# Kernel optimization log

Measured on AMD Instinct MI355X. Metric: run time of the kernel, lower is better.

Reference implementation:

```python
import jax, jax.numpy as jnp
import numpy as np

N_EMBD = 1024
N_HEAD = 16


def setup_inputs() -> dict:
    key = jax.random.key(0)
    ks = jax.random.split(key, 9)
    s = 1.0 / np.sqrt(N_EMBD)
    d = {
        "x": jax.random.normal(ks[0], (4, 2048, N_EMBD), dtype=jnp.float32),
        "Wq": jax.random.normal(ks[1], (N_EMBD, N_EMBD), dtype=jnp.float32) * s,
        "bq": jnp.zeros((N_EMBD,), dtype=jnp.float32),
        "Wk": jax.random.normal(ks[2], (N_EMBD, N_EMBD), dtype=jnp.float32) * s,
        "bk": jnp.zeros((N_EMBD,), dtype=jnp.float32),
        "Wv": jax.random.normal(ks[3], (N_EMBD, N_EMBD), dtype=jnp.float32) * s,
        "bv": jnp.zeros((N_EMBD,), dtype=jnp.float32),
        "Wp": jax.random.normal(ks[4], (N_EMBD, N_EMBD), dtype=jnp.float32) * s,
        "bp": jnp.zeros((N_EMBD,), dtype=jnp.float32),
    }
    return d


def reference(x, Wq, bq, Wk, bk, Wv, bv, Wp, bp):
    B, T, C = x.shape
    H = N_HEAD
    D = C // H  # head dim
    # QKV projections -> [B, H, T, D]
    def split_heads(y):
        return y.reshape(B, T, H, D).transpose(0, 2, 1, 3)
    q = split_heads(x @ Wq + bq)
    k = split_heads(x @ Wk + bk)
    v = split_heads(x @ Wv + bv)
    # full (non-causal) attention, scaled by 1/sqrt(D)
    att = jnp.einsum("bhtd,bhsd->bhts", q, k) * (1.0 / np.sqrt(D))
    att = jax.nn.softmax(att, axis=-1)  # dropout is identity (p=0 / eval)
    out = jnp.einsum("bhts,bhsd->bhtd", att, v)
    out = out.transpose(0, 2, 1, 3).reshape(B, T, C)
    return out @ Wp + bp
```

## Files before the change

### kernel.cpp

```cpp
#include <hip/hip_runtime.h>
#include <math.h>

#define B_ 4
#define T_ 2048
#define C_ 1024
#define H_ 16
#define D_ 64
#define M_ (B_ * T_)

#define QSCALE 0.18033688011112042f

using bf16x8 = __attribute__((ext_vector_type(8))) short;
using f32x4  = __attribute__((ext_vector_type(4))) float;

__device__ __forceinline__ unsigned short f2bf(float f) {
  unsigned u = __float_as_uint(f);
  unsigned r = u + 0x7FFFu + ((u >> 16) & 1u);
  return (unsigned short)(r >> 16);
}
__device__ __forceinline__ float bf2f(unsigned short h) {
  return __uint_as_float(((unsigned)h) << 16);
}
__device__ __forceinline__ unsigned cvtpk_bf16(float lo, float hi) {
  unsigned r;
  asm volatile("v_cvt_pk_bf16_f32 %0, %1, %2" : "=v"(r) : "v"(lo), "v"(hi));
  return r;
}

__global__ __launch_bounds__(256) void conv_x(const float* __restrict__ x,
                                              unsigned short* __restrict__ hi,
                                              unsigned short* __restrict__ lo) {
  const size_t i = ((size_t)blockIdx.x * 256 + threadIdx.x) * 4;
  const float4 v = *(const float4*)&x[i];
  ushort4 h, l;
  h.x = f2bf(v.x); l.x = f2bf(v.x - bf2f(h.x));
  h.y = f2bf(v.y); l.y = f2bf(v.y - bf2f(h.y));
  h.z = f2bf(v.z); l.z = f2bf(v.z - bf2f(h.z));
  h.w = f2bf(v.w); l.w = f2bf(v.w - bf2f(h.w));
  *(ushort4*)&hi[i] = h;
  *(ushort4*)&lo[i] = l;
}

__global__ __launch_bounds__(256) void conv_wT(const float* __restrict__ W,
                                               unsigned short* __restrict__ hi,
                                               unsigned short* __restrict__ lo,
                                               int n_off) {
  __shared__ float t[64][65];
  const int k0 = blockIdx.y * 64, n0 = blockIdx.x * 64;
  const int lr = threadIdx.x >> 4;
  const int lc4 = (threadIdx.x & 15) * 4;
#pragma unroll
  for (int i = 0; i < 4; ++i) {
    const int r = lr + 16 * i;
    const float4 v = *(const float4*)&W[(size_t)(k0 + r) * 1024 + n0 + lc4];
    t[r][lc4 + 0] = v.x; t[r][lc4 + 1] = v.y;
    t[r][lc4 + 2] = v.z; t[r][lc4 + 3] = v.w;
  }
  __syncthreads();
#pragma unroll
  for (int i = 0; i < 4; ++i) {
    const int nr = lr + 16 * i;
    ushort4 h, l;
    float a0 = t[lc4 + 0][nr], a1 = t[lc4 + 1][nr];
    float a2 = t[lc4 + 2][nr], a3 = t[lc4 + 3][nr];
    h.x = f2bf(a0); l.x = f2bf(a0 - bf2f(h.x));
    h.y = f2bf(a1); l.y = f2bf(a1 - bf2f(h.y));
    h.z = f2bf(a2); l.z = f2bf(a2 - bf2f(h.z));
    h.w = f2bf(a3); l.w = f2bf(a3 - bf2f(h.w));
    const size_t o = (size_t)(n_off + n0 + nr) * 1024 + k0 + lc4;
    *(ushort4*)&hi[o] = h;
    *(ushort4*)&lo[o] = l;
  }
}

template <int MODE>
__global__ __launch_bounds__(256) void gemm_mfma(
    const unsigned short* __restrict__ Ahi, const unsigned short* __restrict__ Alo,
    const unsigned short* __restrict__ Bhi, const unsigned short* __restrict__ Blo,
    const float* __restrict__ bias0, const float* __restrict__ bias1,
    const float* __restrict__ bias2,
    void* P0, void* P1, void* P2, void* P3, void* P4, void* P5) {
  __shared__ __align__(16) unsigned short AhS[128 * 32];
  __shared__ __align__(16) unsigned short AlS[128 * 32];
  __shared__ __align__(16) unsigned short BhS[128 * 32];
  __shared__ __align__(16) unsigned short BlS[128 * 32];

  const int tid = threadIdx.x;
  const int lane = tid & 63;
  const int wid = tid >> 6;

  const int GX = (MODE == 1) ? 24 : 8;
  const int nwg = GX * 64;
  int lin = blockIdx.x + blockIdx.y * GX;
  lin = (lin & 7) * (nwg >> 3) + (lin >> 3);
  const int m0 = (lin / GX) * 128, n0 = (lin % GX) * 128;

  const int wm = (wid >> 1) * 64, wn = (wid & 1) * 64;

  f32x4 acc[4][4] = {};

  const int srow = lane >> 2;
  const int sc = lane & 3;
  const int fr = lane & 15;
  const int q = lane >> 4;

  for (int k0 = 0; k0 < 1024; k0 += 32) {
    __syncthreads();
#pragma unroll
    for (int c = 0; c < 2; ++c) {
      const int chunk = wid * 2 + c;
      const int row = chunk * 16 + srow;
      const int kch = sc ^ ((row >> 1) & 3);
      const size_t ao = (size_t)(m0 + row) * 1024 + k0 + kch * 8;
      const size_t bo = (size_t)(n0 + row) * 1024 + k0 + kch * 8;
      __builtin_amdgcn_global_load_lds(
          (const __attribute__((address_space(1))) void*)(Ahi + ao),
          (__attribute__((address_space(3))) void*)(AhS + chunk * 512), 16, 0, 0);
      __builtin_amdgcn_global_load_lds(
          (const __attribute__((address_space(1))) void*)(Alo + ao),
          (__attribute__((address_space(3))) void*)(AlS + chunk * 512), 16, 0, 0);
      __builtin_amdgcn_global_load_lds(
          (const __attribute__((address_space(1))) void*)(Bhi + bo),
          (__attribute__((address_space(3))) void*)(BhS + chunk * 512), 16, 0, 0);
      __builtin_amdgcn_global_load_lds(
          (const __attribute__((address_space(1))) void*)(Blo + bo),
          (__attribute__((address_space(3))) void*)(BlS + chunk * 512), 16, 0, 0);
    }
    __syncthreads();

    bf16x8 afh[4], bfh[4], afl[4], bfl[4];
#pragma unroll
    for (int i = 0; i < 4; ++i) {
      const int arow = wm + i * 16 + fr;
      const int aoff = arow * 32 + (q ^ ((arow >> 1) & 3)) * 8;
      afh[i] = *(const bf16x8*)(AhS + aoff);
      const int brow = wn + i * 16 + fr;
      const int boff = brow * 32 + (q ^ ((brow >> 1) & 3)) * 8;
      bfh[i] = *(const bf16x8*)(BhS + boff);
    }
#pragma unroll
    for (int i = 0; i < 4; ++i)
#pragma unroll
      for (int j = 0; j < 4; ++j)
        acc[i][j] = __builtin_amdgcn_mfma_f32_16x16x32_bf16(afh[i], bfh[j], acc[i][j], 0, 0, 0);
#pragma unroll
    for (int i = 0; i < 4; ++i) {
      const int brow = wn + i * 16 + fr;
      bfl[i] = *(const bf16x8*)(BlS + brow * 32 + (q ^ ((brow >> 1) & 3)) * 8);
    }
#pragma unroll
    for (int i = 0; i < 4; ++i)
#pragma unroll
      for (int j = 0; j < 4; ++j)
        acc[i][j] = __builtin_amdgcn_mfma_f32_16x16x32_bf16(afh[i], bfl[j], acc[i][j], 0, 0, 0);
#pragma unroll
    for (int i = 0; i < 4; ++i) {
      const int arow = wm + i * 16 + fr;
      afl[i] = *(const bf16x8*)(AlS + arow * 32 + (q ^ ((arow >> 1) & 3)) * 8);
    }
#pragma unroll
    for (int i = 0; i < 4; ++i)
#pragma unroll
      for (int j = 0; j < 4; ++j)
        acc[i][j] = __builtin_amdgcn_mfma_f32_16x16x32_bf16(afl[i], bfh[j], acc[i][j], 0, 0, 0);
  }

  if (MODE == 0) {
    float* out = (float*)P0;
#pragma unroll
    for (int i = 0; i < 4; ++i)
#pragma unroll
      for (int j = 0; j < 4; ++j)
#pragma unroll
        for (int r = 0; r < 4; ++r) {
          const int m = m0 + wm + i * 16 + q * 4 + r;
          const int n = n0 + wn + j * 16 + fr;
          out[(size_t)m * 1024 + n] = acc[i][j][r] + bias0[n];
        }
  } else {
#pragma unroll
    for (int i = 0; i < 4; ++i) {
#pragma unroll
      for (int j = 0; j < 4; ++j) {
        const int n = n0 + wn + j * 16 + fr;
        const int seg = n >> 10, ww = n & 1023, h = ww >> 6, d = ww & 63;
        const float bv = ((seg == 0) ? bias0 : (seg == 1) ? bias1 : bias2)[ww];
        const int mb = m0 + wm + i * 16 + q * 4;
        const int b = mb >> 11, t0 = mb & 2047;
        unsigned short hv[4], lv[4];
#pragma unroll
        for (int r = 0; r < 4; ++r) {
          float v = acc[i][j][r] + bv;
          if (seg == 0) v *= QSCALE;
          hv[r] = f2bf(v);
          lv[r] = f2bf(v - bf2f(hv[r]));
        }
        if (seg == 2) {
          const size_t o = (((size_t)b * H_ + h) * D_ + d) * T_ + t0;
          ushort4 h4, l4;
          h4.x = hv[0]; h4.y = hv[1]; h4.z = hv[2]; h4.w = hv[3];
          l4.x = lv[0]; l4.y = lv[1]; l4.z = lv[2]; l4.w = lv[3];
          *(ushort4*)&((unsigned short*)P4)[o] = h4;
          *(ushort4*)&((unsigned short*)P5)[o] = l4;
        } else {
          unsigned short* Hq = (unsigned short*)((seg == 0) ? P0 : P2);
          unsigned short* Lq = (unsigned short*)((seg == 0) ? P1 : P3);
          const size_t ob = ((size_t)b * H_ + h) * T_;
#pragma unroll
          for (int r = 0; r < 4; ++r) {
            const size_t o = (ob + t0 + r) * D_ + d;
            Hq[o] = hv[r];
            Lq[o] = lv[r];
          }
        }
      }
    }
  }
}

__global__ __launch_bounds__(256) void flash_mfma(
    const unsigned short* __restrict__ Qhi, const unsigned short* __restrict__ Qlo,
    const unsigned short* __restrict__ Khi, const unsigned short* __restrict__ Klo,
    const unsigned short* __restrict__ Vthi, const unsigned short* __restrict__ Vtlo,
    unsigned short* __restrict__ chi, unsigned short* __restrict__ clo) {
  __shared__ __align__(16) unsigned short KhiS[2][64 * 64];
  __shared__ __align__(16) unsigned short KloS[2][64 * 64];
  __shared__ __align__(16) unsigned short VhiS[2][64 * 64];
  __shared__ __align__(16) unsigned short VloS[2][64 * 64];
  __shared__ __align__(16) unsigned short PsT[4][32 * 64];

  const int tid = threadIdx.x;
  const int lane = tid & 63;
  const int w = tid >> 6;

  int lin = blockIdx.x + blockIdx.y * 16;
  lin = (lin & 7) * 128 + (lin >> 3);
  const int bh = lin >> 4;
  const int q0 = (lin & 15) * 128;

  const int b = bh >> 4, h = bh & 15;
  const int fr = lane & 15, q = lane >> 4;

  const size_t kbase = (size_t)bh * T_ * D_;
  const size_t vbase = (size_t)bh * D_ * T_;

  const int ci0 = w * 128 + lane;
  const int srow0 = ci0 >> 3, sslot0 = ci0 & 7;
  const int skch0 = sslot0 ^ (srow0 & 7);
  const int ci1 = ci0 + 64;
  const int srow1 = ci1 >> 3, sslot1 = ci1 & 7;
  const int skch1 = sslot1 ^ (srow1 & 7);
  const int ldsb0 = (w * 128) * 8;
  const int ldsb1 = (w * 128 + 64) * 8;

#define STAGE_TILE(buf, s0)                                                      \
  do {                                                                           \
    const unsigned short* k0p = Khi + kbase + (size_t)((s0) + srow0) * D_ + skch0 * 8; \
    const unsigned short* k1p = Klo + kbase + (size_t)((s0) + srow0) * D_ + skch0 * 8; \
    const unsigned short* v0p = Vthi + vbase + (size_t)srow0 * T_ + (s0) + skch0 * 8;  \
    const unsigned short* v1p = Vtlo + vbase + (size_t)srow0 * T_ + (s0) + skch0 * 8;  \
    __builtin_amdgcn_global_load_lds(                                            \
        (const __attribute__((address_space(1))) void*)k0p,                      \
        (__attribute__((address_space(3))) void*)(KhiS[buf] + ldsb0), 16, 0, 0); \
    __builtin_amdgcn_global_load_lds(                                            \
        (const __attribute__((address_space(1))) void*)k1p,                      \
        (__attribute__((address_space(3))) void*)(KloS[buf] + ldsb0), 16, 0, 0); \
    __builtin_amdgcn_global_load_lds(                                            \
        (const __attribute__((address_space(1))) void*)v0p,                      \
        (__attribute__((address_space(3))) void*)(VhiS[buf] + ldsb0), 16, 0, 0); \
    __builtin_amdgcn_global_load_lds(                                            \
        (const __attribute__((address_space(1))) void*)v1p,                      \
        (__attribute__((address_space(3))) void*)(VloS[buf] + ldsb0), 16, 0, 0); \
    const unsigned short* k2p = Khi + kbase + (size_t)((s0) + srow1) * D_ + skch1 * 8; \
    const unsigned short* k3p = Klo + kbase + (size_t)((s0) + srow1) * D_ + skch1 * 8; \
    const unsigned short* v2p = Vthi + vbase + (size_t)srow1 * T_ + (s0) + skch1 * 8;  \
    const unsigned short* v3p = Vtlo + vbase + (size_t)srow1 * T_ + (s0) + skch1 * 8;  \
    __builtin_amdgcn_global_load_lds(                                            \
        (const __attribute__((address_space(1))) void*)k2p,                      \
        (__attribute__((address_space(3))) void*)(KhiS[buf] + ldsb1), 16, 0, 0); \
    __builtin_amdgcn_global_load_lds(                                            \
        (const __attribute__((address_space(1))) void*)k3p,                      \
        (__attribute__((address_space(3))) void*)(KloS[buf] + ldsb1), 16, 0, 0); \
    __builtin_amdgcn_global_load_lds(                                            \
        (const __attribute__((address_space(1))) void*)v2p,                      \
        (__attribute__((address_space(3))) void*)(VhiS[buf] + ldsb1), 16, 0, 0); \
    __builtin_amdgcn_global_load_lds(                                            \
        (const __attribute__((address_space(1))) void*)v3p,                      \
        (__attribute__((address_space(3))) void*)(VloS[buf] + ldsb1), 16, 0, 0); \
  } while (0)

  bf16x8 qhi[2][2], qlo[2][2];
#pragma unroll
  for (int g = 0; g < 2; ++g)
#pragma unroll
    for (int ks = 0; ks < 2; ++ks) {
      const size_t a = kbase + (size_t)(q0 + w * 32 + g * 16 + fr) * D_ + ks * 32 + q * 8;
      qhi[g][ks] = *(const bf16x8*)(Qhi + a);
      qlo[g][ks] = *(const bf16x8*)(Qlo + a);
    }

  unsigned short* psw = &PsT[w][0];

  f32x4 accO[4][2] = {};
  float lsum[2] = {};

  STAGE_TILE(0, 0);

  int cur = 0;
  for (int s0 = 0; s0 < T_; s0 += 64) {
    const bool more = (s0 + 64) < T_;
    if (more) {
      STAGE_TILE(cur ^ 1, s0 + 64);
      asm volatile("s_waitcnt vmcnt(8)" ::: "memory");
    } else {
      asm volatile("s_waitcnt vmcnt(0)" ::: "memory");
    }
    __builtin_amdgcn_sched_barrier(0);
    asm volatile("s_barrier" ::: "memory");
    __builtin_amdgcn_sched_barrier(0);

    const unsigned short* KhS = KhiS[cur];
    const unsigned short* KlS = KloS[cur];
    const unsigned short* VhS = VhiS[cur];
    const unsigned short* VlS = VloS[cur];

    f32x4 accS[4][2] = {};
#pragma unroll
    for (int sj = 0; sj < 4; ++sj) {
      bf16x8 khf[2], klf[2];
#pragma unroll
      for (int ks = 0; ks < 2; ++ks) {
        const int rs = sj * 16 + fr;
        const int off = rs * 64 + ((ks * 4 + q) ^ (rs & 7)) * 8;
        khf[ks] = *(const bf16x8*)(KhS + off);
        klf[ks] = *(const bf16x8*)(KlS + off);
      }
#pragma unroll
      for (int g = 0; g < 2; ++g)
#pragma unroll
        for (int ks = 0; ks < 2; ++ks) {
          accS[sj][g] = __builtin_amdgcn_mfma_f32_16x16x32_bf16(khf[ks], qhi[g][ks], accS[sj][g], 0, 0, 0);
          accS[sj][g] = __builtin_amdgcn_mfma_f32_16x16x32_bf16(khf[ks], qlo[g][ks], accS[sj][g], 0, 0, 0);
          accS[sj][g] = __builtin_amdgcn_mfma_f32_16x16x32_bf16(klf[ks], qhi[g][ks], accS[sj][g], 0, 0, 0);
        }
    }

#pragma unroll
    for (int g = 0; g < 2; ++g) {
      const int qc = g * 16 + fr;
#pragma unroll
      for (int sj = 0; sj < 4; ++sj) {
        const float p0 = __builtin_amdgcn_exp2f(accS[sj][g][0]);
        const float p1 = __builtin_amdgcn_exp2f(accS[sj][g][1]);
        const float p2 = __builtin_amdgcn_exp2f(accS[sj][g][2]);
        const float p3 = __builtin_amdgcn_exp2f(accS[sj][g][3]);
        lsum[g] += (p0 + p1) + (p2 + p3);
        uint2 pk;
        pk.x = cvtpk_bf16(p0, p1);
        pk.y = cvtpk_bf16(p2, p3);
        const int off = (qc * 128 + sj * 32 + q * 8) ^ ((fr & 7) << 4);
        *(uint2*)((char*)psw + off) = pk;
      }
    }

    asm volatile("s_waitcnt lgkmcnt(0)" ::: "memory");
    __builtin_amdgcn_sched_barrier(0);

    bf16x8 pb[2][2];
#pragma unroll
    for (int g = 0; g < 2; ++g)
#pragma unroll
      for (int ks = 0; ks < 2; ++ks) {
        const int off = ((g * 16 + fr) * 128 + ks * 64 + q * 16) ^ ((fr & 7) << 4);
        pb[g][ks] = *(const bf16x8*)((char*)psw + off);
      }
#pragma unroll
    for (int j = 0; j < 4; ++j) {
      bf16x8 vh[2], vl[2];
#pragma unroll
      for (int ks = 0; ks < 2; ++ks) {
        const int rd = j * 16 + fr;
        const int off = rd * 64 + ((ks * 4 + q) ^ (rd & 7)) * 8;
        vh[ks] = *(const bf16x8*)(VhS + off);
        vl[ks] = *(const bf16x8*)(VlS + off);
      }
#pragma unroll
      for (int g = 0; g < 2; ++g)
#pragma unroll
        for (int ks = 0; ks < 2; ++ks) {
          accO[j][g] = __builtin_amdgcn_mfma_f32_16x16x32_bf16(vh[ks], pb[g][ks], accO[j][g], 0, 0, 0);
          accO[j][g] = __builtin_amdgcn_mfma_f32_16x16x32_bf16(vl[ks], pb[g][ks], accO[j][g], 0, 0, 0);
        }
    }

    __builtin_amdgcn_sched_barrier(0);
    asm volatile("s_barrier" ::: "memory");
    __builtin_amdgcn_sched_barrier(0);
    cur ^= 1;
  }

#pragma unroll
  for (int g = 0; g < 2; ++g) {
    float rs = lsum[g];
    rs += __shfl_xor(rs, 16);
    rs += __shfl_xor(rs, 32);
    const float inv = 1.0f / rs;
    const int t = q0 + w * 32 + g * 16 + fr;
    const size_t rowb = ((size_t)b * T_ + t) * C_ + h * D_;
#pragma unroll
    for (int j = 0; j < 4; ++j) {
      ushort4 h4, l4;
      float v0 = accO[j][g][0] * inv, v1 = accO[j][g][1] * inv;
      float v2 = accO[j][g][2] * inv, v3 = accO[j][g][3] * inv;
      h4.x = f2bf(v0); l4.x = f2bf(v0 - bf2f(h4.x));
      h4.y = f2bf(v1); l4.y = f2bf(v1 - bf2f(h4.y));
      h4.z = f2bf(v2); l4.z = f2bf(v2 - bf2f(h4.z));
      h4.w = f2bf(v3); l4.w = f2bf(v3 - bf2f(h4.w));
      const size_t idx = rowb + j * 16 + q * 4;
      *(ushort4*)&chi[idx] = h4;
      *(ushort4*)&clo[idx] = l4;
    }
  }
#undef STAGE_TILE
}

extern "C" void kernel_launch(void* const* d_in, const int* in_sizes, int n_in,
                              void* d_out, int out_size, void* d_ws,
                              size_t ws_size, hipStream_t stream) {
  const float* x = (const float*)d_in[0];
  const float* Wq = (const float*)d_in[1];
  const float* bq = (const float*)d_in[2];
  const float* Wk = (const float*)d_in[3];
  const float* bk = (const float*)d_in[4];
  const float* Wv = (const float*)d_in[5];
  const float* bv = (const float*)d_in[6];
  const float* Wp = (const float*)d_in[7];
  const float* bp = (const float*)d_in[8];
  float* out = (float*)d_out;

  char* w = (char*)d_ws;
  unsigned short* xhi = (unsigned short*)w;     w += (size_t)M_ * C_ * 2;
  unsigned short* xlo = (unsigned short*)w;     w += (size_t)M_ * C_ * 2;
  unsigned short* Wqkv_hi = (unsigned short*)w; w += (size_t)3 * C_ * C_ * 2;
  unsigned short* Wqkv_lo = (unsigned short*)w; w += (size_t)3 * C_ * C_ * 2;
  unsigned short* Wp_hi = (unsigned short*)w;   w += (size_t)C_ * C_ * 2;
  unsigned short* Wp_lo = (unsigned short*)w;   w += (size_t)C_ * C_ * 2;
  unsigned short* Qhi = (unsigned short*)w;     w += (size_t)M_ * C_ * 2;
  unsigned short* Qlo = (unsigned short*)w;     w += (size_t)M_ * C_ * 2;
  unsigned short* Khi = (unsigned short*)w;     w += (size_t)M_ * C_ * 2;
  unsigned short* Klo = (unsigned short*)w;     w += (size_t)M_ * C_ * 2;
  unsigned short* Vthi = (unsigned short*)w;    w += (size_t)M_ * C_ * 2;
  unsigned short* Vtlo = (unsigned short*)w;    w += (size_t)M_ * C_ * 2;
  unsigned short* chi = (unsigned short*)w;     w += (size_t)M_ * C_ * 2;
  unsigned short* clo = (unsigned short*)w;     w += (size_t)M_ * C_ * 2;

  const dim3 blk(256);

  conv_x<<<dim3((M_ * C_) / (4 * 256)), blk, 0, stream>>>(x, xhi, xlo);
  conv_wT<<<dim3(16, 16), blk, 0, stream>>>(Wq, Wqkv_hi, Wqkv_lo, 0);
  conv_wT<<<dim3(16, 16), blk, 0, stream>>>(Wk, Wqkv_hi, Wqkv_lo, 1024);
  conv_wT<<<dim3(16, 16), blk, 0, stream>>>(Wv, Wqkv_hi, Wqkv_lo, 2048);
  conv_wT<<<dim3(16, 16), blk, 0, stream>>>(Wp, Wp_hi, Wp_lo, 0);

  gemm_mfma<1><<<dim3(3072 / 128, M_ / 128), blk, 0, stream>>>(
      xhi, xlo, Wqkv_hi, Wqkv_lo, bq, bk, bv,
      Qhi, Qlo, Khi, Klo, Vthi, Vtlo);

  flash_mfma<<<dim3(T_ / 128, B_ * H_), blk, 0, stream>>>(
      Qhi, Qlo, Khi, Klo, Vthi, Vtlo, chi, clo);

  gemm_mfma<0><<<dim3(1024 / 128, M_ / 128), blk, 0, stream>>>(
      chi, clo, Wp_hi, Wp_lo, bp, bp, bp,
      out, nullptr, nullptr, nullptr, nullptr, nullptr);

  (void)in_sizes; (void)n_in; (void)out_size; (void)ws_size;
}
```

Before: 493.1 us.

## Double-buffer GEMM LDS staging with 256x128 tiles and 8-wave blocks

Reworks the split-bf16 GEMM kernel so each 512-thread block computes a 256x128 output tile. The next K-slice is prefetched into a second LDS buffer while the current one is consumed, with explicit vmcnt waits, barriers and MFMA priority raising. This is meant to hide global-to-LDS load latency behind MFMA work and to raise operand reuse per block. In exchange, LDS use roughly doubles per block, which can lower occupancy, and the extra barriers per K-step add synchronisation cost.

```diff
diff --git a/kernel.cpp b/kernel.cpp
--- a/kernel.cpp
+++ b/kernel.cpp
@@ -74,95 +74,137 @@
 }
 
 template <int MODE>
-__global__ __launch_bounds__(256) void gemm_mfma(
+__global__ __launch_bounds__(512, 2) void gemm_mfma(
     const unsigned short* __restrict__ Ahi, const unsigned short* __restrict__ Alo,
     const unsigned short* __restrict__ Bhi, const unsigned short* __restrict__ Blo,
     const float* __restrict__ bias0, const float* __restrict__ bias1,
     const float* __restrict__ bias2,
     void* P0, void* P1, void* P2, void* P3, void* P4, void* P5) {
-  __shared__ __align__(16) unsigned short AhS[128 * 32];
-  __shared__ __align__(16) unsigned short AlS[128 * 32];
-  __shared__ __align__(16) unsigned short BhS[128 * 32];
-  __shared__ __align__(16) unsigned short BlS[128 * 32];
+  __shared__ __align__(16) unsigned short AhS[2][256 * 32];
+  __shared__ __align__(16) unsigned short AlS[2][256 * 32];
+  __shared__ __align__(16) unsigned short BhS[2][128 * 32];
+  __shared__ __align__(16) unsigned short BlS[2][128 * 32];
 
   const int tid = threadIdx.x;
   const int lane = tid & 63;
-  const int wid = tid >> 6;
+  const int w = tid >> 6;
 
   const int GX = (MODE == 1) ? 24 : 8;
-  const int nwg = GX * 64;
+  const int nwg = GX * 32;
   int lin = blockIdx.x + blockIdx.y * GX;
   lin = (lin & 7) * (nwg >> 3) + (lin >> 3);
-  const int m0 = (lin / GX) * 128, n0 = (lin % GX) * 128;
-
-  const int wm = (wid >> 1) * 64, wn = (wid & 1) * 64;
+  const int m0 = (lin / GX) * 256, n0 = (lin % GX) * 128;
+
+  const int wm = (w >> 1) * 64, wn = (w & 1) * 64;
+  const int fr = lane & 15, q = lane >> 4;
+
+  const int ciA0 = w * 64 + lane;
+  const int ciA1 = ciA0 + 512;
+  const int rA0 = ciA0 >> 2, sA0 = (ciA0 & 3) ^ ((rA0 >> 1) & 3);
+  const int rA1 = ciA1 >> 2, sA1 = (ciA1 & 3) ^ ((rA1 >> 1) & 3);
+  const int rB = rA0, sB = sA0;
 
   f32x4 acc[4][4] = {};
 
-  const int srow = lane >> 2;
-  const int sc = lane & 3;
-  const int fr = lane & 15;
-  const int q = lane >> 4;
+  auto stage = [&](int buf, int kk) {
+    const size_t oa0 = (size_t)(m0 + rA0) * 1024 + kk + sA0 * 8;
+    const size_t oa1 = (size_t)(m0 + rA1) * 1024 + kk + sA1 * 8;
+    const size_t ob  = (size_t)(n0 + rB) * 1024 + kk + sB * 8;
+    __builtin_amdgcn_global_load_lds(
+        (const __attribute__((address_space(1))) void*)(Ahi + oa0),
+        (__attribute__((address_space(3))) void*)(&AhS[buf][ciA0 * 8]), 16, 0, 0);
+    __builtin_amdgcn_global_load_lds(
+        (const __attribute__((address_space(1))) void*)(Alo + oa0),
+        (__attribute__((address_space(3))) void*)(&AlS[buf][ciA0 * 8]), 16, 0, 0);
+    __builtin_amdgcn_global_load_lds(
+        (const __attribute__((address_space(1))) void*)(Ahi + oa1),
+        (__attribute__((address_space(3))) void*)(&AhS[buf][ciA1 * 8]), 16, 0, 0);
+    __builtin_amdgcn_global_load_lds(
+        (const __attribute__((address_space(1))) void*)(Alo + oa1),
+        (__attribute__((address_space(3))) void*)(&AlS[buf][ciA1 * 8]), 16, 0, 0);
+    __builtin_amdgcn_global_load_lds(
+        (const __attribute__((address_space(1))) void*)(Bhi + ob),
+        (__attribute__((address_space(3))) void*)(&BhS[buf][ciA0 * 8]), 16, 0, 0);
+    __builtin_amdgcn_global_load_lds(
+        (const __attribute__((address_space(1))) void*)(Blo + ob),
+        (__attribute__((address_space(3))) void*)(&BlS[buf][ciA0 * 8]), 16, 0, 0);
+  };
+
+  auto frag = [&](const unsigned short* arr, int row) {
+    return *(const bf16x8*)(arr + row * 32 + ((q ^ ((row >> 1) & 3)) * 8));
+  };
+
+  stage(0, 0);
+  int cur = 0;
 
   for (int k0 = 0; k0 < 1024; k0 += 32) {
-    __syncthreads();
-#pragma unroll
-    for (int c = 0; c < 2; ++c) {
-      const int chunk = wid * 2 + c;
-      const int row = chunk * 16 + srow;
-      const int kch = sc ^ ((row >> 1) & 3);
-      const size_t ao = (size_t)(m0 + row) * 1024 + k0 + kch * 8;
-      const size_t bo = (size_t)(n0 + row) * 1024 + k0 + kch * 8;
-      __builtin_amdgcn_global_load_lds(
-          (const __attribute__((address_space(1))) void*)(Ahi + ao),
-          (__attribute__((address_space(3))) void*)(AhS + chunk * 512), 16, 0, 0);
-      __builtin_amdgcn_global_load_lds(
-          (const __attribute__((address_space(1))) void*)(Alo + ao),
-          (__attribute__((address_space(3))) void*)(AlS + chunk * 512), 16, 0, 0);
-      __builtin_amdgcn_global_load_lds(
-          (const __attribute__((address_space(1))) void*)(Bhi + bo),
-          (__attribute__((address_space(3))) void*)(BhS + chunk * 512), 16, 0, 0);
-      __builtin_amdgcn_global_load_lds(
-          (const __attribute__((address_space(1))) void*)(Blo + bo),
-          (__attribute__((address_space(3))) void*)(BlS + chunk * 512), 16, 0, 0);
-    }
-    __syncthreads();
-
-    bf16x8 afh[4], bfh[4], afl[4], bfl[4];
-#pragma unroll
-    for (int i = 0; i < 4; ++i) {
-      const int arow = wm + i * 16 + fr;
-      const int aoff = arow * 32 + (q ^ ((arow >> 1) & 3)) * 8;
-      afh[i] = *(const bf16x8*)(AhS + aoff);
-      const int brow = wn + i * 16 + fr;
-      const int boff = brow * 32 + (q ^ ((brow >> 1) & 3)) * 8;
-      bfh[i] = *(const bf16x8*)(BhS + boff);
-    }
+    const bool more = (k0 + 32) < 1024;
+    if (more) {
+      stage(cur ^ 1, k0 + 32);
+      asm volatile("s_waitcnt vmcnt(6)" ::: "memory");
+    } else {
+      asm volatile("s_waitcnt vmcnt(0)" ::: "memory");
+    }
+    __builtin_amdgcn_sched_barrier(0);
+    asm volatile("s_barrier" ::: "memory");
+    __builtin_amdgcn_sched_barrier(0);
+
+    const unsigned short* ah = AhS[cur];
+    const unsigned short* al = AlS[cur];
+    const unsigned short* bh = BhS[cur];
+    const unsigned short* bl = BlS[cur];
+
+    bf16x8 afh[4], bfh[4];
+#pragma unroll
+    for (int i = 0; i < 4; ++i) afh[i] = frag(ah, wm + i * 16 + fr);
+#pragma unroll
+    for (int j = 0; j < 4; ++j) bfh[j] = frag(bh, wn + j * 16 + fr);
+    asm volatile("s_waitcnt lgkmcnt(0)" ::: "memory");
+    __builtin_amdgcn_sched_barrier(0);
+    __builtin_amdgcn_s_setprio(1);
 #pragma unroll
     for (int i = 0; i < 4; ++i)
 #pragma unroll
       for (int j = 0; j < 4; ++j)
         acc[i][j] = __builtin_amdgcn_mfma_f32_16x16x32_bf16(afh[i], bfh[j], acc[i][j], 0, 0, 0);
-#pragma unroll
-    for (int i = 0; i < 4; ++i) {
-      const int brow = wn + i * 16 + fr;
-      bfl[i] = *(const bf16x8*)(BlS + brow * 32 + (q ^ ((brow >> 1) & 3)) * 8);
-    }
+    __builtin_amdgcn_s_setprio(0);
+    __builtin_amdgcn_sched_barrier(0);
+    asm volatile("s_barrier" ::: "memory");
+    __builtin_amdgcn_sched_barrier(0);
+
+    bf16x8 bfl[4];
+#pragma unroll
+    for (int j = 0; j < 4; ++j) bfl[j] = frag(bl, wn + j * 16 + fr);
+    asm volatile("s_waitcnt lgkmcnt(0)" ::: "memory");
+    __builtin_amdgcn_sched_barrier(0);
+    __builtin_amdgcn_s_setprio(1);
 #pragma unroll
     for (int i = 0; i < 4; ++i)
 #pragma unroll
       for (int j = 0; j < 4; ++j)
         acc[i][j] = __builtin_amdgcn_mfma_f32_16x16x32_bf16(afh[i], bfl[j], acc[i][j], 0, 0, 0);
-#pragma unroll
-    for (int i = 0; i < 4; ++i) {
-      const int arow = wm + i * 16 + fr;
-      afl[i] = *(const bf16x8*)(AlS + arow * 32 + (q ^ ((arow >> 1) & 3)) * 8);
-    }
+    __builtin_amdgcn_s_setprio(0);
+    __builtin_amdgcn_sched_barrier(0);
+    asm volatile("s_barrier" ::: "memory");
+    __builtin_amdgcn_sched_barrier(0);
+
+    bf16x8 afl[4];
+#pragma unroll
+    for (int i = 0; i < 4; ++i) afl[i] = frag(al, wm + i * 16 + fr);
+    asm volatile("s_waitcnt lgkmcnt(0)" ::: "memory");
+    __builtin_amdgcn_sched_barrier(0);
+    __builtin_amdgcn_s_setprio(1);
 #pragma unroll
     for (int i = 0; i < 4; ++i)
 #pragma unroll
       for (int j = 0; j < 4; ++j)
         acc[i][j] = __builtin_amdgcn_mfma_f32_16x16x32_bf16(afl[i], bfh[j], acc[i][j], 0, 0, 0);
+    __builtin_amdgcn_s_setprio(0);
+    __builtin_amdgcn_sched_barrier(0);
+    asm volatile("s_barrier" ::: "memory");
+    __builtin_amdgcn_sched_barrier(0);
+
+    cur ^= 1;
   }
 
   if (MODE == 0) {
@@ -455,6 +497,7 @@
   unsigned short* clo = (unsigned short*)w;     w += (size_t)M_ * C_ * 2;
 
   const dim3 blk(256);
+  const dim3 blkg(512);
 
   conv_x<<<dim3((M_ * C_) / (4 * 256)), blk, 0, stream>>>(x, xhi, xlo);
   conv_wT<<<dim3(16, 16), blk, 0, stream>>>(Wq, Wqkv_hi, Wqkv_lo, 0);
@@ -462,14 +505,14 @@
   conv_wT<<<dim3(16, 16), blk, 0, stream>>>(Wv, Wqkv_hi, Wqkv_lo, 2048);
   conv_wT<<<dim3(16, 16), blk, 0, stream>>>(Wp, Wp_hi, Wp_lo, 0);
 
-  gemm_mfma<1><<<dim3(3072 / 128, M_ / 128), blk, 0, stream>>>(
+  gemm_mfma<1><<<dim3(24, 32), blkg, 0, stream>>>(
       xhi, xlo, Wqkv_hi, Wqkv_lo, bq, bk, bv,
       Qhi, Qlo, Khi, Klo, Vthi, Vtlo);
 
   flash_mfma<<<dim3(T_ / 128, B_ * H_), blk, 0, stream>>>(
       Qhi, Qlo, Khi, Klo, Vthi, Vtlo, chi, clo);
 
-  gemm_mfma<0><<<dim3(1024 / 128, M_ / 128), blk, 0, stream>>>(
+  gemm_mfma<0><<<dim3(8, 32), blkg, 0, stream>>>(
       chi, clo, Wp_hi, Wp_lo, bp, bp, bp,
       out, nullptr, nullptr, nullptr, nullptr, nullptr);
 
```

Measured after the change: 518.4 us. +5.1%, slower.
